# Optimization experiments

Hardware: AMD Instinct MI355X
Metric: run time of the kernel (lower is better)

Reference implementation:

```python
import jax, jax.numpy as jnp
import numpy as np

B, S, V, E, H, XD, C = 64, 512, 32000, 512, 1024, 512, 1024


def setup_inputs() -> dict:
    key = jax.random.key(0)
    ks = jax.random.split(key, 20)
    s = 0.02
    inp = {
        "X": jax.random.randint(ks[0], (B, S), 0, V),
        "h0": jax.random.normal(ks[1], (B, H), jnp.float32),
        "embed": jax.random.normal(ks[2], (V, E), jnp.float32) * s,
        "Wzh": jax.random.normal(ks[3], (H, H), jnp.float32) * s,
        "bzh": jnp.zeros((H,), jnp.float32),
        "Wzx": jax.random.normal(ks[4], (H, E), jnp.float32) * s,
        "bzx": jnp.zeros((H,), jnp.float32),
        "Wrh": jax.random.normal(ks[5], (H, H), jnp.float32) * s,
        "brh": jnp.zeros((H,), jnp.float32),
        "Wrx": jax.random.normal(ks[6], (H, E), jnp.float32) * s,
        "brx": jnp.zeros((H,), jnp.float32),
        "Wuh": jax.random.normal(ks[7], (H, H), jnp.float32) * s,
        "buh": jnp.zeros((H,), jnp.float32),
        "Wux": jax.random.normal(ks[8], (H, E), jnp.float32) * s,
        "bux": jnp.zeros((H,), jnp.float32),
        "Wxh": jax.random.normal(ks[9], (XD, H), jnp.float32) * s,
        "bxh": jnp.zeros((XD,), jnp.float32),
        "Wc": jax.random.normal(ks[10], (C, XD), jnp.float32) * s,
        "bc": jnp.zeros((C,), jnp.float32),
    }
    return inp


def reference(X, h0, embed, Wzh, bzh, Wzx, bzx, Wrh, brh, Wrx, brx,
              Wuh, buh, Wux, bux, Wxh, bxh, Wc, bc):
    x_embed = embed[X]                    # [B,S,E]
    xs = jnp.transpose(x_embed, (1, 0, 2))  # [S,B,E] for scan

    def step(ht, xt):
        zt = jax.nn.sigmoid(ht @ Wzh.T + bzh + xt @ Wzx.T + bzx)
        rt = jax.nn.sigmoid(ht @ Wrh.T + brh + xt @ Wrx.T + brx)
        ht_cand = jnp.tanh((rt * ht) @ Wuh.T + buh + xt @ Wux.T + bux)
        ht_new = (1.0 - zt) * ht + zt * ht_cand
        yt = ht_new @ Wxh.T + bxh          # [B,XD]
        yprob = yt @ Wc.T + bc             # [B,C]
        return ht_new, yprob

    _, yprobs = jax.lax.scan(step, h0, xs)  # [S,B,C]
    return jnp.transpose(yprobs, (1, 0, 2))  # [B,S,C]
```

## Files before the change

kernel.cpp:

```cpp
#include <hip/hip_runtime.h>

#define DEV __device__ __forceinline__

using bf16x8 = __attribute__((ext_vector_type(8))) short;
using u16x4  = __attribute__((ext_vector_type(4))) unsigned short;
using f32x4  = __attribute__((ext_vector_type(4))) float;

constexpr int B_ = 64, S_ = 512, V_ = 32000, E_ = 512, H_ = 1024, C_ = 1024;
constexpr int NWG = 128;
constexpr int JS  = 8;

constexpr size_t OFF_FH    = 0;
constexpr size_t OFF_FR    = 512;
constexpr size_t OFF_BIASG = 1024;
constexpr size_t OFF_BCOMB = OFF_BIASG + 3072*4;
constexpr size_t OFF_HB    = OFF_BCOMB + 1024*4;
constexpr size_t OFF_RHB   = OFF_HB + (size_t)B_*H_*2;
constexpr size_t OFF_WCOMB = OFF_RHB + (size_t)B_*H_*2;
constexpr size_t OFF_WXALL = OFF_WCOMB + (size_t)C_*H_*2;
constexpr size_t OFF_WZRF  = OFF_WXALL + (size_t)3072*512*2;
constexpr size_t OFF_WUF   = OFF_WZRF + (size_t)NWG*32768;
constexpr size_t OFF_EMB   = OFF_WUF + (size_t)NWG*16384;
constexpr size_t OFF_G     = OFF_EMB + (size_t)V_*E_*2;
constexpr size_t OFF_HS    = OFF_G + (size_t)S_*B_*3072*2;
constexpr size_t WS_NEED   = OFF_HS + (size_t)S_*B_*H_*2;

DEV unsigned short f2bf(float f){
  unsigned int x; __builtin_memcpy(&x, &f, 4);
  x += 0x7fffu + ((x>>16)&1u);
  return (unsigned short)(x>>16);
}
DEV float bf2f(unsigned short u){
  unsigned int x = ((unsigned int)u)<<16; float f; __builtin_memcpy(&f,&x,4); return f;
}

DEV int4 ld16_coh(const char* p){
  int4 r;
  asm volatile("global_load_dwordx4 %0, %1, off sc0 sc1" : "=v"(r) : "v"(p) : "memory");
  return r;
}
DEV void st16_coh(char* p, bf16x8 v){
  asm volatile("global_store_dwordx4 %0, %1, off sc0 sc1" :: "v"(p), "v"(v) : "memory");
}
DEV uint2 ld8_plain(const char* p){
  uint2 r;
  asm volatile("global_load_dwordx2 %0, %1, off" : "=v"(r) : "v"(p) : "memory");
  return r;
}

#define WAITVM(N) do{ asm volatile("s_waitcnt vmcnt(" #N ")" ::: "memory"); \
                      __builtin_amdgcn_sched_barrier(0); }while(0)

__global__ void k_cvt_embed(const float* __restrict__ src, unsigned short* __restrict__ dst){
  for (int i = blockIdx.x*blockDim.x + threadIdx.x; i < V_*E_; i += gridDim.x*blockDim.x)
    dst[i] = f2bf(src[i]);
}

__global__ void k_build_wx(const float* __restrict__ Wzx, const float* __restrict__ Wrx,
                           const float* __restrict__ Wux, unsigned short* __restrict__ out){
  for (int i = blockIdx.x*blockDim.x + threadIdx.x; i < 3072*512; i += gridDim.x*blockDim.x){
    int n = i>>9, k = i&511;
    int g = n>>10, r = n&1023;
    const float* W = (g==0) ? Wzx : (g==1) ? Wrx : Wux;
    out[i] = f2bf(W[(size_t)r*512 + k]);
  }
}

__global__ void k_biasg(const float* bzh, const float* bzx, const float* brh, const float* brx,
                        const float* buh, const float* bux, float* __restrict__ out){
  for (int i = blockIdx.x*blockDim.x + threadIdx.x; i < 3072; i += gridDim.x*blockDim.x){
    int g = i>>10, r = i&1023;
    float v = (g==0) ? (bzh[r]+bzx[r]) : (g==1) ? (brh[r]+brx[r]) : (buh[r]+bux[r]);
    out[i] = v;
  }
}

__global__ void k_frag(const float* __restrict__ Wa, const float* __restrict__ Wb,
                       unsigned short* __restrict__ out){
  for (int i = blockIdx.x*blockDim.x + threadIdx.x; i < NWG*32*64*8; i += gridDim.x*blockDim.x){
    int e  = i & 7;
    int l  = (i>>3) & 63;
    int ck = (i>>9) & 31;
    int wg = i>>14;
    int j  = l & 15;
    int k  = ck*32 + ((l>>4)<<3) + e;
    int row = wg*JS + (j&7);
    float v = (j < 8) ? Wa[(size_t)row*H_ + k] : Wb[(size_t)row*H_ + k];
    out[i] = f2bf(v);
  }
}

__global__ void k_frag2(const float* __restrict__ Wuh, unsigned short* __restrict__ out){
  for (int i = blockIdx.x*blockDim.x + threadIdx.x; i < NWG*32*32*8; i += gridDim.x*blockDim.x){
    int e=i&7, p=(i>>3)&31, ck=(i>>8)&31, wg=i>>13;
    int nn=p&7, h8=p>>3;
    out[i] = f2bf(Wuh[(size_t)(wg*8+nn)*H_ + ck*32 + h8*8 + e]);
  }
}

__global__ __launch_bounds__(256) void k_wcomb(const float* __restrict__ Wc,
                                               const float* __restrict__ Wxh,
                                               unsigned short* __restrict__ Wcomb){
  __shared__ float wc[16][512];
  const int c0 = blockIdx.x*16;
  const int tid = threadIdx.x;
  for (int q = tid; q < 16*512; q += 256)
    wc[q>>9][q&511] = Wc[(size_t)(c0 + (q>>9))*512 + (q&511)];
  __syncthreads();
  const int h4 = tid*4;
  f32x4 acc[16];
  #pragma unroll
  for (int ci=0; ci<16; ++ci) acc[ci] = (f32x4){0.f,0.f,0.f,0.f};
  for (int x=0; x<512; ++x){
    f32x4 wv = *(const f32x4*)(Wxh + (size_t)x*H_ + h4);
    #pragma unroll
    for (int ci=0; ci<16; ++ci) acc[ci] += wc[ci][x] * wv;
  }
  #pragma unroll
  for (int ci=0; ci<16; ++ci)
    #pragma unroll
    for (int e=0; e<4; ++e)
      Wcomb[(size_t)(c0+ci)*H_ + h4 + e] = f2bf(acc[ci][e]);
}

__global__ void k_bcomb(const float* __restrict__ Wc, const float* __restrict__ bxh,
                        const float* __restrict__ bc, float* __restrict__ out){
  int c = blockIdx.x*blockDim.x + threadIdx.x;
  if (c >= C_) return;
  float s = bc[c];
  for (int x=0; x<512; ++x) s += Wc[(size_t)c*512 + x]*bxh[x];
  out[c] = s;
}

__global__ void k_hinit(const float* __restrict__ h0, unsigned short* __restrict__ hbF){
  int i = blockIdx.x*256 + threadIdx.x;
  int e=i&7, l=(i>>3)&63, ck=(i>>9)&31, w=i>>14;
  hbF[i] = f2bf(h0[(size_t)(w*16+(l&15))*H_ + ck*32 + ((l>>4)<<3) + e]);
}

template<bool GATHER, int MODE>
__global__ __launch_bounds__(256) void gemm_bt(
  const unsigned short* __restrict__ Asrc, const int* __restrict__ Xidx,
  const unsigned short* __restrict__ embB,
  const unsigned short* __restrict__ Bw, const float* __restrict__ bias,
  void* __restrict__ Cout, int K, int KT, int NTN, int ldc)
{
  __shared__ unsigned short ldsA[128*64];
  __shared__ unsigned short ldsB[128*64];
  const int bid = blockIdx.x;
  const int tm = bid / NTN, tn = bid % NTN;
  const int m0 = tm*128, n0 = tn*128;
  const int tid = threadIdx.x, wave = tid>>6, lane = tid&63;
  const int wm = (wave&1)*64, wn = (wave>>1)*64;

  const char* srcA[4]; const char* srcB[4];
  int rr[4], cc[4];
  #pragma unroll
  for (int s=0; s<4; ++s){
    int L = s*4096 + tid*16;
    int r = L>>7, cb = L&127;
    rr[s]=r; cc[s]=cb;
    if constexpr (GATHER){
      int m = m0 + r; int tt = m>>6, bb = m&63;
      srcA[s] = (const char*)(embB + (size_t)Xidx[bb*S_ + tt]*(size_t)K);
    } else {
      srcA[s] = (const char*)(Asrc + (size_t)(m0+r)*(size_t)K);
    }
    srcB[s] = (const char*)(Bw + (size_t)(n0+r)*(size_t)K);
  }

  f32x4 acc[4][4];
  #pragma unroll
  for (int a=0;a<4;a++)
    #pragma unroll
    for (int b=0;b<4;b++) acc[a][b] = (f32x4){0.f,0.f,0.f,0.f};

  int4 ra[4], rb[4];
  auto loadRegs = [&](int kt){
    #pragma unroll
    for (int s=0;s<4;s++){
      ra[s] = *(const int4*)(srcA[s] + (size_t)kt*128 + cc[s]);
      rb[s] = *(const int4*)(srcB[s] + (size_t)kt*128 + cc[s]);
    }
  };
  auto writeLDS = [&](){
    #pragma unroll
    for (int s=0;s<4;s++){
      int off = (rr[s]<<7) + (cc[s] ^ ((rr[s]&7)<<4));
      *(int4*)((char*)ldsA + off) = ra[s];
      *(int4*)((char*)ldsB + off) = rb[s];
    }
  };

  loadRegs(0);
  for (int kt=0; kt<KT; ++kt){
    __syncthreads();
    writeLDS();
    if (kt+1 < KT) loadRegs(kt+1);
    __syncthreads();
    #pragma unroll
    for (int ck=0; ck<2; ++ck){
      bf16x8 af[4], bfr[4];
      #pragma unroll
      for (int q=0;q<4;q++){
        int ar = wm + q*16 + (lane&15);
        int ao = (ar<<7) + (((ck<<6) + ((lane>>4)<<4)) ^ ((ar&7)<<4));
        af[q] = *(const bf16x8*)((const char*)ldsA + ao);
        int br = wn + q*16 + (lane&15);
        int bo = (br<<7) + (((ck<<6) + ((lane>>4)<<4)) ^ ((br&7)<<4));
        bfr[q] = *(const bf16x8*)((const char*)ldsB + bo);
      }
      #pragma unroll
      for (int mi=0;mi<4;mi++)
        #pragma unroll
        for (int ni=0;ni<4;ni++)
          acc[mi][ni] = __builtin_amdgcn_mfma_f32_16x16x32_bf16(af[mi], bfr[ni], acc[mi][ni], 0,0,0);
    }
  }

  #pragma unroll
  for (int mi=0;mi<4;mi++){
    #pragma unroll
    for (int ni=0;ni<4;ni++){
      int gm = m0 + wm + mi*16 + ((lane>>4)<<2);
      int gn = n0 + wn + ni*16 + (lane&15);
      float bv = bias[gn];
      if constexpr (MODE == 1){
        #pragma unroll
        for (int r2=0;r2<4;r2++){
          float v = acc[mi][ni][r2] + bv;
          int m = gm + r2;
          ((float*)Cout)[ (size_t)((m&63)*S_ + (m>>6))*(size_t)ldc + gn ] = v;
        }
      } else {
        int t0 = gm>>6, b0 = gm&63;
        u16x4 pk;
        #pragma unroll
        for (int r2=0;r2<4;r2++) pk[r2] = f2bf(acc[mi][ni][r2] + bv);
        *(u16x4*)((unsigned short*)Cout + ((size_t)t0*3072 + gn)*64 + b0) = pk;
      }
    }
  }
}

DEV void pollge(const unsigned int* f, unsigned int p, int lane){
  const unsigned long long* q = (const unsigned long long*)f;
  int guard = 0;
  for(;;){
    unsigned long long v = __hip_atomic_load(&q[lane], __ATOMIC_RELAXED, __HIP_MEMORY_SCOPE_AGENT);
    bool ok = ((unsigned)v >= p) && ((unsigned)(v>>32) >= p);
    if (__all((int)ok)) break;
    __builtin_amdgcn_s_sleep(1);
    if (++guard > (1<<22)) break;
  }
}

__global__ __launch_bounds__(256) void k_scan(const float* __restrict__ h0, char* __restrict__ ws){
  const int wg = blockIdx.x;
  const int tid = threadIdx.x;
  const int wave = tid>>6, lane = tid&63;
  const int j0 = wg*JS;
  const int ckw = wg>>2, hiw = wg&3;

  unsigned int* fH = (unsigned int*)(ws + OFF_FH);
  unsigned int* fR = (unsigned int*)(ws + OFF_FR);
  char* hbF  = ws + OFF_HB;
  char* rhbF = ws + OFF_RHB;
  const unsigned short* G = (const unsigned short*)(ws + OFF_G);
  unsigned short* Hs  = (unsigned short*)(ws + OFF_HS);

  __shared__ __align__(16) char lds[32768 + 16384 + 1024 + 1024];
  char* f1  = lds;
  char* f2p = lds + 32768;
  unsigned short* tileA = (unsigned short*)(lds + 49152);
  unsigned short* tileB = (unsigned short*)(lds + 50176);

  {
    const int4* s1 = (const int4*)(ws + OFF_WZRF + (size_t)wg*32768);
    const int4* s2 = (const int4*)(ws + OFF_WUF  + (size_t)wg*16384);
    #pragma unroll
    for (int i=0;i<8;i++) ((int4*)f1)[tid + i*256] = s1[tid + i*256];
    #pragma unroll
    for (int i=0;i<4;i++) ((int4*)f2p)[tid + i*256] = s2[tid + i*256];
  }
  __syncthreads();

  const int n  = lane & 15;
  const int c  = n & 7;
  const bool isZ = (n < 8);
  const int hi2 = lane>>4;
  const int rbase = (wave<<4) + (hi2<<2);
  const int gcol = ((n>>3)<<10) + j0 + c;
  const int col2 = 2048 + j0 + c;

  float h_own[4];
  #pragma unroll
  for (int r2=0;r2<4;r2++)
    h_own[r2] = isZ ? h0[(size_t)(rbase+r2)*H_ + j0 + c] : 0.f;

  const char* myHb  = hbF  + ((size_t)wave<<15);
  const char* myRhb = rhbF + ((size_t)wave<<15);

#define LOAD8(buf, base, g0) { _Pragma("unroll") \
  for (int i=0;i<8;i++) buf[i] = ld16_coh((base) + ((((g0)*8+i)*64+lane)<<4)); }
#define MFMA8_1(buf, g0) { _Pragma("unroll") \
  for (int i=0;i<8;i++){ int ck=(g0)*8+i; \
    bf16x8 bv = *(const bf16x8*)(f1 + ((ck*64+lane)<<4)); \
    bf16x8 av = __builtin_bit_cast(bf16x8, buf[i]); \
    if (i&1) acc1 = __builtin_amdgcn_mfma_f32_16x16x32_bf16(av,bv,acc1,0,0,0); \
    else     acc0 = __builtin_amdgcn_mfma_f32_16x16x32_bf16(av,bv,acc0,0,0,0);} }
#define MFMA8_2(buf, g0) { _Pragma("unroll") \
  for (int i=0;i<8;i++){ int ck=(g0)*8+i; \
    bf16x8 bv = *(const bf16x8*)(f2p + ((ck*32 + hi2*8 + c)<<4)); \
    bf16x8 av = __builtin_bit_cast(bf16x8, buf[i]); \
    if (i&1) acc1 = __builtin_amdgcn_mfma_f32_16x16x32_bf16(av,bv,acc1,0,0,0); \
    else     acc0 = __builtin_amdgcn_mfma_f32_16x16x32_bf16(av,bv,acc0,0,0,0);} }

  for (int t=0; t<S_; ++t){
    uint2 gv1 = ld8_plain((const char*)(G + ((size_t)t*3072 + gcol)*64 + rbase));
    uint2 gv2 = ld8_plain((const char*)(G + ((size_t)t*3072 + col2)*64 + rbase));

    if (t > 0) pollge(fH, (unsigned)t, lane);
    WAITVM(0);

    f32x4 acc0 = (f32x4){0,0,0,0}, acc1 = (f32x4){0,0,0,0};
    {
      int4 bufA[8], bufB[8];
      LOAD8(bufA, myHb, 0);
      LOAD8(bufB, myHb, 1); WAITVM(8); MFMA8_1(bufA, 0);
      LOAD8(bufA, myHb, 2); WAITVM(8); MFMA8_1(bufB, 1);
      LOAD8(bufB, myHb, 3); WAITVM(8); MFMA8_1(bufA, 2);
      WAITVM(0);            MFMA8_1(bufB, 3);
    }
    f32x4 accs = acc0 + acc1;

    float zval[4];
    {
      unsigned short gu[4] = {(unsigned short)(gv1.x&0xffffu),(unsigned short)(gv1.x>>16),
                              (unsigned short)(gv1.y&0xffffu),(unsigned short)(gv1.y>>16)};
      #pragma unroll
      for (int r2=0;r2<4;r2++){
        float pre = accs[r2] + bf2f(gu[r2]);
        float sv = 1.f/(1.f + __expf(-pre));
        float hc = __shfl(h_own[r2], (lane & 48) | c, 64);
        zval[r2] = sv;
        if (!isZ) tileA[(wave*16 + hi2*4 + r2)*8 + c] = f2bf(sv*hc);
      }
    }
    __syncthreads();
    if (wave == 0){
      bf16x8 v = *(const bf16x8*)(tileA + lane*8);
      st16_coh(rhbF + ((((lane>>4)*32 + ckw)<<10) + (hiw<<8) + ((lane&15)<<4)), v);
      asm volatile("s_waitcnt vmcnt(0)" ::: "memory");
      if (lane == 0)
        __hip_atomic_store(&fR[wg], (unsigned)(t+1), __ATOMIC_RELAXED, __HIP_MEMORY_SCOPE_AGENT);
    }
    pollge(fR, (unsigned)(t+1), lane);
    WAITVM(0);

    acc0 = (f32x4){0,0,0,0}; acc1 = (f32x4){0,0,0,0};
    {
      int4 bufA[8], bufB[8];
      LOAD8(bufA, myRhb, 0);
      LOAD8(bufB, myRhb, 1); WAITVM(8); MFMA8_2(bufA, 0);
      LOAD8(bufA, myRhb, 2); WAITVM(8); MFMA8_2(bufB, 1);
      LOAD8(bufB, myRhb, 3); WAITVM(8); MFMA8_2(bufA, 2);
      WAITVM(0);             MFMA8_2(bufB, 3);
    }
    f32x4 acc2 = acc0 + acc1;

    if (isZ){
      unsigned short gu[4] = {(unsigned short)(gv2.x&0xffffu),(unsigned short)(gv2.x>>16),
                              (unsigned short)(gv2.y&0xffffu),(unsigned short)(gv2.y>>16)};
      #pragma unroll
      for (int r2=0;r2<4;r2++){
        float up = acc2[r2] + bf2f(gu[r2]);
        float e  = __expf(-2.f*up);
        float u  = (1.f - e)/(1.f + e);
        float hn = h_own[r2] + zval[r2]*(u - h_own[r2]);
        h_own[r2] = hn;
        tileB[(wave*16 + hi2*4 + r2)*8 + c] = f2bf(hn);
      }
    }
    __syncthreads();
    if (wave == 0){
      bf16x8 v = *(const bf16x8*)(tileB + lane*8);
      st16_coh(hbF + ((((lane>>4)*32 + ckw)<<10) + (hiw<<8) + ((lane&15)<<4)), v);
      *(bf16x8*)(Hs + (size_t)((t<<6) + lane)*H_ + j0) = v;
      asm volatile("s_waitcnt vmcnt(0)" ::: "memory");
      if (lane == 0)
        __hip_atomic_store(&fH[wg], (unsigned)(t+1), __ATOMIC_RELAXED, __HIP_MEMORY_SCOPE_AGENT);
    }
  }
#undef LOAD8
#undef MFMA8_1
#undef MFMA8_2
}

extern "C" void kernel_launch(void* const* d_in, const int* in_sizes, int n_in,
                              void* d_out, int out_size, void* d_ws, size_t ws_size,
                              hipStream_t stream)
{
  const int*   X    = (const int*)  d_in[0];
  const float* h0   = (const float*)d_in[1];
  const float* emb  = (const float*)d_in[2];
  const float* Wzh  = (const float*)d_in[3];
  const float* bzh  = (const float*)d_in[4];
  const float* Wzx  = (const float*)d_in[5];
  const float* bzx  = (const float*)d_in[6];
  const float* Wrh  = (const float*)d_in[7];
  const float* brh  = (const float*)d_in[8];
  const float* Wrx  = (const float*)d_in[9];
  const float* brx  = (const float*)d_in[10];
  const float* Wuh  = (const float*)d_in[11];
  const float* buh  = (const float*)d_in[12];
  const float* Wux  = (const float*)d_in[13];
  const float* bux  = (const float*)d_in[14];
  const float* Wxh  = (const float*)d_in[15];
  const float* bxh  = (const float*)d_in[16];
  const float* Wc   = (const float*)d_in[17];
  const float* bc   = (const float*)d_in[18];
  (void)in_sizes; (void)n_in;

  char* ws = (char*)d_ws;
  if (ws_size < WS_NEED){
    hipMemsetAsync(d_out, 0, (size_t)out_size*4, stream);
    return;
  }

  hipMemsetAsync(ws + OFF_FH, 0, 1024, stream);

  k_cvt_embed<<<4096, 256, 0, stream>>>(emb, (unsigned short*)(ws + OFF_EMB));
  k_build_wx <<<1536, 256, 0, stream>>>(Wzx, Wrx, Wux, (unsigned short*)(ws + OFF_WXALL));
  k_biasg    <<<12,   256, 0, stream>>>(bzh, bzx, brh, brx, buh, bux, (float*)(ws + OFF_BIASG));
  k_frag     <<<2048, 256, 0, stream>>>(Wzh, Wrh, (unsigned short*)(ws + OFF_WZRF));
  k_frag2    <<<1024, 256, 0, stream>>>(Wuh,      (unsigned short*)(ws + OFF_WUF));
  k_wcomb    <<<64,   256, 0, stream>>>(Wc, Wxh, (unsigned short*)(ws + OFF_WCOMB));
  k_bcomb    <<<4,    256, 0, stream>>>(Wc, bxh, bc, (float*)(ws + OFF_BCOMB));
  k_hinit    <<<256,  256, 0, stream>>>(h0, (unsigned short*)(ws + OFF_HB));

  gemm_bt<true,2><<<6144, 256, 0, stream>>>(
      nullptr, X, (const unsigned short*)(ws + OFF_EMB),
      (const unsigned short*)(ws + OFF_WXALL), (const float*)(ws + OFF_BIASG),
      (void*)(ws + OFF_G), 512, 8, 24, 3072);

  k_scan<<<NWG, 256, 0, stream>>>(h0, ws);

  gemm_bt<false,1><<<2048, 256, 0, stream>>>(
      (const unsigned short*)(ws + OFF_HS), nullptr, nullptr,
      (const unsigned short*)(ws + OFF_WCOMB), (const float*)(ws + OFF_BCOMB),
      d_out, 1024, 16, 8, 1024);
}
```

Measured before the change: 6.754 ms.

## Split scan into 512 single-wave workgroups with independent batch-quarter sync groups

The recurrent scan kernel goes from 128 four-wave workgroups to 512 single-wave workgroups, one per (column group, batch quarter). Each batch quarter now has its own flags and hidden-state buffers, so groups synchronise only with the 128 workgroups sharing their 16 batch rows. This removes the intra-block __syncthreads and the wave-0 serialised store, and shrinks each barrier's fan-in. In exchange each workgroup reloads the full 48KB weight fragment into LDS (4x total LDS footprint), and more workgroups spin-poll flags, which may increase memory traffic and require co-residency of 512 blocks.

```diff
diff --git a/kernel.cpp b/kernel.cpp
--- a/kernel.cpp
+++ b/kernel.cpp
@@ -7,20 +7,21 @@
 using f32x4  = __attribute__((ext_vector_type(4))) float;
 
 constexpr int B_ = 64, S_ = 512, V_ = 32000, E_ = 512, H_ = 1024, C_ = 1024;
-constexpr int NWG = 128;
+constexpr int NCG = 128;
+constexpr int NBG = 4;
 constexpr int JS  = 8;
 
 constexpr size_t OFF_FH    = 0;
-constexpr size_t OFF_FR    = 512;
-constexpr size_t OFF_BIASG = 1024;
+constexpr size_t OFF_FR    = 2048;
+constexpr size_t OFF_BIASG = 4096;
 constexpr size_t OFF_BCOMB = OFF_BIASG + 3072*4;
 constexpr size_t OFF_HB    = OFF_BCOMB + 1024*4;
-constexpr size_t OFF_RHB   = OFF_HB + (size_t)B_*H_*2;
-constexpr size_t OFF_WCOMB = OFF_RHB + (size_t)B_*H_*2;
+constexpr size_t OFF_RHB   = OFF_HB + (size_t)4*32768;
+constexpr size_t OFF_WCOMB = OFF_RHB + (size_t)4*32768;
 constexpr size_t OFF_WXALL = OFF_WCOMB + (size_t)C_*H_*2;
 constexpr size_t OFF_WZRF  = OFF_WXALL + (size_t)3072*512*2;
-constexpr size_t OFF_WUF   = OFF_WZRF + (size_t)NWG*32768;
-constexpr size_t OFF_EMB   = OFF_WUF + (size_t)NWG*16384;
+constexpr size_t OFF_WUF   = OFF_WZRF + (size_t)NCG*32768;
+constexpr size_t OFF_EMB   = OFF_WUF + (size_t)NCG*16384;
 constexpr size_t OFF_G     = OFF_EMB + (size_t)V_*E_*2;
 constexpr size_t OFF_HS    = OFF_G + (size_t)S_*B_*3072*2;
 constexpr size_t WS_NEED   = OFF_HS + (size_t)S_*B_*H_*2;
@@ -77,24 +78,24 @@
 
 __global__ void k_frag(const float* __restrict__ Wa, const float* __restrict__ Wb,
                        unsigned short* __restrict__ out){
-  for (int i = blockIdx.x*blockDim.x + threadIdx.x; i < NWG*32*64*8; i += gridDim.x*blockDim.x){
+  for (int i = blockIdx.x*blockDim.x + threadIdx.x; i < NCG*32*64*8; i += gridDim.x*blockDim.x){
     int e  = i & 7;
     int l  = (i>>3) & 63;
     int ck = (i>>9) & 31;
-    int wg = i>>14;
+    int g  = i>>14;
     int j  = l & 15;
     int k  = ck*32 + ((l>>4)<<3) + e;
-    int row = wg*JS + (j&7);
+    int row = g*JS + (j&7);
     float v = (j < 8) ? Wa[(size_t)row*H_ + k] : Wb[(size_t)row*H_ + k];
     out[i] = f2bf(v);
   }
 }
 
 __global__ void k_frag2(const float* __restrict__ Wuh, unsigned short* __restrict__ out){
-  for (int i = blockIdx.x*blockDim.x + threadIdx.x; i < NWG*32*32*8; i += gridDim.x*blockDim.x){
-    int e=i&7, p=(i>>3)&31, ck=(i>>8)&31, wg=i>>13;
+  for (int i = blockIdx.x*blockDim.x + threadIdx.x; i < NCG*32*32*8; i += gridDim.x*blockDim.x){
+    int e=i&7, p=(i>>3)&31, ck=(i>>8)&31, g=i>>13;
     int nn=p&7, h8=p>>3;
-    out[i] = f2bf(Wuh[(size_t)(wg*8+nn)*H_ + ck*32 + h8*8 + e]);
+    out[i] = f2bf(Wuh[(size_t)(g*8+nn)*H_ + ck*32 + h8*8 + e]);
   }
 }
 
@@ -134,8 +135,8 @@
 
 __global__ void k_hinit(const float* __restrict__ h0, unsigned short* __restrict__ hbF){
   int i = blockIdx.x*256 + threadIdx.x;
-  int e=i&7, l=(i>>3)&63, ck=(i>>9)&31, w=i>>14;
-  hbF[i] = f2bf(h0[(size_t)(w*16+(l&15))*H_ + ck*32 + ((l>>4)<<3) + e]);
+  int e=i&7, l=(i>>3)&63, ck=(i>>9)&31, q=i>>14;
+  hbF[i] = f2bf(h0[(size_t)(q*16+(l&15))*H_ + ck*32 + ((l>>4)<<3) + e]);
 }
 
 template<bool GATHER, int MODE>
@@ -255,41 +256,42 @@
   }
 }
 
-__global__ __launch_bounds__(256) void k_scan(const float* __restrict__ h0, char* __restrict__ ws){
-  const int wg = blockIdx.x;
-  const int tid = threadIdx.x;
-  const int wave = tid>>6, lane = tid&63;
-  const int j0 = wg*JS;
-  const int ckw = wg>>2, hiw = wg&3;
-
-  unsigned int* fH = (unsigned int*)(ws + OFF_FH);
-  unsigned int* fR = (unsigned int*)(ws + OFF_FR);
-  char* hbF  = ws + OFF_HB;
-  char* rhbF = ws + OFF_RHB;
+__global__ __launch_bounds__(64) void k_scan(const float* __restrict__ h0, char* __restrict__ ws){
+  const int Wid = blockIdx.x;
+  const int g = Wid & 127;
+  const int q = Wid >> 7;
+  const int lane = threadIdx.x;
+  const int j0 = g*JS;
+  const int b0 = q*16;
+
+  unsigned int* fH = (unsigned int*)(ws + OFF_FH) + q*128;
+  unsigned int* fR = (unsigned int*)(ws + OFF_FR) + q*128;
+  char* HF  = ws + OFF_HB  + (size_t)q*32768;
+  char* RHF = ws + OFF_RHB + (size_t)q*32768;
   const unsigned short* G = (const unsigned short*)(ws + OFF_G);
   unsigned short* Hs  = (unsigned short*)(ws + OFF_HS);
 
-  __shared__ __align__(16) char lds[32768 + 16384 + 1024 + 1024];
+  __shared__ __align__(16) char lds[32768 + 16384 + 512];
   char* f1  = lds;
   char* f2p = lds + 32768;
-  unsigned short* tileA = (unsigned short*)(lds + 49152);
-  unsigned short* tileB = (unsigned short*)(lds + 50176);
+  unsigned short* tA = (unsigned short*)(lds + 49152);
+  unsigned short* tB = (unsigned short*)(lds + 49152 + 256);
 
   {
-    const int4* s1 = (const int4*)(ws + OFF_WZRF + (size_t)wg*32768);
-    const int4* s2 = (const int4*)(ws + OFF_WUF  + (size_t)wg*16384);
-    #pragma unroll
-    for (int i=0;i<8;i++) ((int4*)f1)[tid + i*256] = s1[tid + i*256];
-    #pragma unroll
-    for (int i=0;i<4;i++) ((int4*)f2p)[tid + i*256] = s2[tid + i*256];
-  }
-  __syncthreads();
-
-  const int n  = lane & 15;
-  const int c  = n & 7;
+    const int4* s1 = (const int4*)(ws + OFF_WZRF + (size_t)g*32768);
+    const int4* s2 = (const int4*)(ws + OFF_WUF  + (size_t)g*16384);
+    #pragma unroll
+    for (int i=0;i<32;i++) ((int4*)f1)[lane + i*64]  = s1[lane + i*64];
+    #pragma unroll
+    for (int i=0;i<16;i++) ((int4*)f2p)[lane + i*64] = s2[lane + i*64];
+  }
+  asm volatile("s_waitcnt lgkmcnt(0)" ::: "memory");
+
+  const int n   = lane & 15;
+  const int c   = lane & 7;
   const bool isZ = (n < 8);
-  const int hi2 = lane>>4;
-  const int rbase = (wave<<4) + (hi2<<2);
+  const int hi4 = lane >> 4;
+  const int rbase = b0 + hi4*4;
   const int gcol = ((n>>3)<<10) + j0 + c;
   const int col2 = 2048 + j0 + c;
 
@@ -297,9 +299,6 @@
   #pragma unroll
   for (int r2=0;r2<4;r2++)
     h_own[r2] = isZ ? h0[(size_t)(rbase+r2)*H_ + j0 + c] : 0.f;
-
-  const char* myHb  = hbF  + ((size_t)wave<<15);
-  const char* myRhb = rhbF + ((size_t)wave<<15);
 
 #define LOAD8(buf, base, g0) { _Pragma("unroll") \
   for (int i=0;i<8;i++) buf[i] = ld16_coh((base) + ((((g0)*8+i)*64+lane)<<4)); }
@@ -311,7 +310,7 @@
     else     acc0 = __builtin_amdgcn_mfma_f32_16x16x32_bf16(av,bv,acc0,0,0,0);} }
 #define MFMA8_2(buf, g0) { _Pragma("unroll") \
   for (int i=0;i<8;i++){ int ck=(g0)*8+i; \
-    bf16x8 bv = *(const bf16x8*)(f2p + ((ck*32 + hi2*8 + c)<<4)); \
+    bf16x8 bv = *(const bf16x8*)(f2p + ((ck*32 + hi4*8 + c)<<4)); \
     bf16x8 av = __builtin_bit_cast(bf16x8, buf[i]); \
     if (i&1) acc1 = __builtin_amdgcn_mfma_f32_16x16x32_bf16(av,bv,acc1,0,0,0); \
     else     acc0 = __builtin_amdgcn_mfma_f32_16x16x32_bf16(av,bv,acc0,0,0,0);} }
@@ -321,16 +320,15 @@
     uint2 gv2 = ld8_plain((const char*)(G + ((size_t)t*3072 + col2)*64 + rbase));
 
     if (t > 0) pollge(fH, (unsigned)t, lane);
-    WAITVM(0);
 
     f32x4 acc0 = (f32x4){0,0,0,0}, acc1 = (f32x4){0,0,0,0};
     {
       int4 bufA[8], bufB[8];
-      LOAD8(bufA, myHb, 0);
-      LOAD8(bufB, myHb, 1); WAITVM(8); MFMA8_1(bufA, 0);
-      LOAD8(bufA, myHb, 2); WAITVM(8); MFMA8_1(bufB, 1);
-      LOAD8(bufB, myHb, 3); WAITVM(8); MFMA8_1(bufA, 2);
-      WAITVM(0);            MFMA8_1(bufB, 3);
+      LOAD8(bufA, HF, 0);
+      LOAD8(bufB, HF, 1); WAITVM(8); MFMA8_1(bufA, 0);
+      LOAD8(bufA, HF, 2); WAITVM(8); MFMA8_1(bufB, 1);
+      LOAD8(bufB, HF, 3); WAITVM(8); MFMA8_1(bufA, 2);
+      WAITVM(0);          MFMA8_1(bufB, 3);
     }
     f32x4 accs = acc0 + acc1;
 
@@ -342,30 +340,30 @@
       for (int r2=0;r2<4;r2++){
         float pre = accs[r2] + bf2f(gu[r2]);
         float sv = 1.f/(1.f + __expf(-pre));
-        float hc = __shfl(h_own[r2], (lane & 48) | c, 64);
+        float hc = __shfl_xor(h_own[r2], 8, 64);
         zval[r2] = sv;
-        if (!isZ) tileA[(wave*16 + hi2*4 + r2)*8 + c] = f2bf(sv*hc);
+        if (!isZ) tA[(hi4*4+r2)*8 + c] = f2bf(sv*hc);
       }
     }
-    __syncthreads();
-    if (wave == 0){
-      bf16x8 v = *(const bf16x8*)(tileA + lane*8);
-      st16_coh(rhbF + ((((lane>>4)*32 + ckw)<<10) + (hiw<<8) + ((lane&15)<<4)), v);
-      asm volatile("s_waitcnt vmcnt(0)" ::: "memory");
-      if (lane == 0)
-        __hip_atomic_store(&fR[wg], (unsigned)(t+1), __ATOMIC_RELAXED, __HIP_MEMORY_SCOPE_AGENT);
-    }
+    asm volatile("s_waitcnt lgkmcnt(0)" ::: "memory");
+    __builtin_amdgcn_sched_barrier(0);
+    if (lane < 16){
+      bf16x8 v = *(const bf16x8*)(tA + lane*8);
+      st16_coh(RHF + g*256 + lane*16, v);
+    }
+    WAITVM(0);
+    if (lane == 0)
+      __hip_atomic_store(&fR[g], (unsigned)(t+1), __ATOMIC_RELAXED, __HIP_MEMORY_SCOPE_AGENT);
     pollge(fR, (unsigned)(t+1), lane);
-    WAITVM(0);
 
     acc0 = (f32x4){0,0,0,0}; acc1 = (f32x4){0,0,0,0};
     {
       int4 bufA[8], bufB[8];
-      LOAD8(bufA, myRhb, 0);
-      LOAD8(bufB, myRhb, 1); WAITVM(8); MFMA8_2(bufA, 0);
-      LOAD8(bufA, myRhb, 2); WAITVM(8); MFMA8_2(bufB, 1);
-      LOAD8(bufB, myRhb, 3); WAITVM(8); MFMA8_2(bufA, 2);
-      WAITVM(0);             MFMA8_2(bufB, 3);
+      LOAD8(bufA, RHF, 0);
+      LOAD8(bufB, RHF, 1); WAITVM(8); MFMA8_2(bufA, 0);
+      LOAD8(bufA, RHF, 2); WAITVM(8); MFMA8_2(bufB, 1);
+      LOAD8(bufB, RHF, 3); WAITVM(8); MFMA8_2(bufA, 2);
+      WAITVM(0);           MFMA8_2(bufB, 3);
     }
     f32x4 acc2 = acc0 + acc1;
 
@@ -379,18 +377,19 @@
         float u  = (1.f - e)/(1.f + e);
         float hn = h_own[r2] + zval[r2]*(u - h_own[r2]);
         h_own[r2] = hn;
-        tileB[(wave*16 + hi2*4 + r2)*8 + c] = f2bf(hn);
+        tB[(hi4*4+r2)*8 + c] = f2bf(hn);
       }
     }
-    __syncthreads();
-    if (wave == 0){
-      bf16x8 v = *(const bf16x8*)(tileB + lane*8);
-      st16_coh(hbF + ((((lane>>4)*32 + ckw)<<10) + (hiw<<8) + ((lane&15)<<4)), v);
-      *(bf16x8*)(Hs + (size_t)((t<<6) + lane)*H_ + j0) = v;
-      asm volatile("s_waitcnt vmcnt(0)" ::: "memory");
-      if (lane == 0)
-        __hip_atomic_store(&fH[wg], (unsigned)(t+1), __ATOMIC_RELAXED, __HIP_MEMORY_SCOPE_AGENT);
-    }
+    asm volatile("s_waitcnt lgkmcnt(0)" ::: "memory");
+    __builtin_amdgcn_sched_barrier(0);
+    if (lane < 16){
+      bf16x8 v = *(const bf16x8*)(tB + lane*8);
+      *(bf16x8*)(Hs + (size_t)((t<<6) + b0 + lane)*H_ + j0) = v;
+      st16_coh(HF + g*256 + lane*16, v);
+    }
+    WAITVM(0);
+    if (lane == 0)
+      __hip_atomic_store(&fH[g], (unsigned)(t+1), __ATOMIC_RELAXED, __HIP_MEMORY_SCOPE_AGENT);
   }
 #undef LOAD8
 #undef MFMA8_1
@@ -428,7 +427,7 @@
     return;
   }
 
-  hipMemsetAsync(ws + OFF_FH, 0, 1024, stream);
+  hipMemsetAsync(ws + OFF_FH, 0, 4096, stream);
 
   k_cvt_embed<<<4096, 256, 0, stream>>>(emb, (unsigned short*)(ws + OFF_EMB));
   k_build_wx <<<1536, 256, 0, stream>>>(Wzx, Wrx, Wux, (unsigned short*)(ws + OFF_WXALL));
@@ -444,7 +443,7 @@
       (const unsigned short*)(ws + OFF_WXALL), (const float*)(ws + OFF_BIASG),
       (void*)(ws + OFF_G), 512, 8, 24, 3072);
 
-  k_scan<<<NWG, 256, 0, stream>>>(h0, ws);
+  k_scan<<<NCG*NBG, 64, 0, stream>>>(h0, ws);
 
   gemm_bt<false,1><<<2048, 256, 0, stream>>>(
       (const unsigned short*)(ws + OFF_HS), nullptr, nullptr,
```

After: 8.558 ms. +26.7%, slower.

## Replace block barriers with per-wave publishing and fetch-add counter flags

Applied to the files above, without the earlier changes.

Each wave now writes its own 16 rows of r*h and h to private LDS slices and publishes them to global memory itself. Each wave then bumps the workgroup flag with an atomic fetch-add, and pollers wait for four increments per step. This removes the two __syncthreads per timestep and the single-wave publish bottleneck. The change also issues all 32 coherent loads up front with staged waits, splits the MFMA chain across four accumulators, removes s_sleep from the poll loop and sets launch_bounds occupancy to 1. The cost is more atomics, more register pressure and busier polling traffic.

```diff
diff --git a/kernel.cpp b/kernel.cpp
--- a/kernel.cpp
+++ b/kernel.cpp
@@ -50,6 +50,8 @@
 
 #define WAITVM(N) do{ asm volatile("s_waitcnt vmcnt(" #N ")" ::: "memory"); \
                       __builtin_amdgcn_sched_barrier(0); }while(0)
+#define WAITLGKM() do{ asm volatile("s_waitcnt lgkmcnt(0)" ::: "memory"); \
+                       __builtin_amdgcn_sched_barrier(0); }while(0)
 
 __global__ void k_cvt_embed(const float* __restrict__ src, unsigned short* __restrict__ dst){
   for (int i = blockIdx.x*blockDim.x + threadIdx.x; i < V_*E_; i += gridDim.x*blockDim.x)
@@ -250,12 +252,11 @@
     unsigned long long v = __hip_atomic_load(&q[lane], __ATOMIC_RELAXED, __HIP_MEMORY_SCOPE_AGENT);
     bool ok = ((unsigned)v >= p) && ((unsigned)(v>>32) >= p);
     if (__all((int)ok)) break;
-    __builtin_amdgcn_s_sleep(1);
-    if (++guard > (1<<22)) break;
-  }
-}
-
-__global__ __launch_bounds__(256) void k_scan(const float* __restrict__ h0, char* __restrict__ ws){
+    if (++guard > (1<<24)) break;
+  }
+}
+
+__global__ __launch_bounds__(256,1) void k_scan(const float* __restrict__ h0, char* __restrict__ ws){
   const int wg = blockIdx.x;
   const int tid = threadIdx.x;
   const int wave = tid>>6, lane = tid&63;
@@ -269,11 +270,11 @@
   const unsigned short* G = (const unsigned short*)(ws + OFF_G);
   unsigned short* Hs  = (unsigned short*)(ws + OFF_HS);
 
-  __shared__ __align__(16) char lds[32768 + 16384 + 1024 + 1024];
+  __shared__ __align__(16) char lds[32768 + 16384 + 2048];
   char* f1  = lds;
   char* f2p = lds + 32768;
-  unsigned short* tileA = (unsigned short*)(lds + 49152);
-  unsigned short* tileB = (unsigned short*)(lds + 50176);
+  unsigned short* tAw = (unsigned short*)(lds + 49152 + wave*256);
+  unsigned short* tBw = (unsigned short*)(lds + 49152 + 1024 + wave*256);
 
   {
     const int4* s1 = (const int4*)(ws + OFF_WZRF + (size_t)wg*32768);
@@ -300,6 +301,8 @@
 
   const char* myHb  = hbF  + ((size_t)wave<<15);
   const char* myRhb = rhbF + ((size_t)wave<<15);
+  char* pubR = rhbF + ((size_t)wave<<15) + ((size_t)ckw<<10) + (hiw<<8);
+  char* pubH = hbF  + ((size_t)wave<<15) + ((size_t)ckw<<10) + (hiw<<8);
 
 #define LOAD8(buf, base, g0) { _Pragma("unroll") \
   for (int i=0;i<8;i++) buf[i] = ld16_coh((base) + ((((g0)*8+i)*64+lane)<<4)); }
@@ -307,32 +310,31 @@
   for (int i=0;i<8;i++){ int ck=(g0)*8+i; \
     bf16x8 bv = *(const bf16x8*)(f1 + ((ck*64+lane)<<4)); \
     bf16x8 av = __builtin_bit_cast(bf16x8, buf[i]); \
-    if (i&1) acc1 = __builtin_amdgcn_mfma_f32_16x16x32_bf16(av,bv,acc1,0,0,0); \
-    else     acc0 = __builtin_amdgcn_mfma_f32_16x16x32_bf16(av,bv,acc0,0,0,0);} }
+    accv[i&3] = __builtin_amdgcn_mfma_f32_16x16x32_bf16(av,bv,accv[i&3],0,0,0);} }
 #define MFMA8_2(buf, g0) { _Pragma("unroll") \
   for (int i=0;i<8;i++){ int ck=(g0)*8+i; \
     bf16x8 bv = *(const bf16x8*)(f2p + ((ck*32 + hi2*8 + c)<<4)); \
     bf16x8 av = __builtin_bit_cast(bf16x8, buf[i]); \
-    if (i&1) acc1 = __builtin_amdgcn_mfma_f32_16x16x32_bf16(av,bv,acc1,0,0,0); \
-    else     acc0 = __builtin_amdgcn_mfma_f32_16x16x32_bf16(av,bv,acc0,0,0,0);} }
+    accv[i&3] = __builtin_amdgcn_mfma_f32_16x16x32_bf16(av,bv,accv[i&3],0,0,0);} }
 
   for (int t=0; t<S_; ++t){
     uint2 gv1 = ld8_plain((const char*)(G + ((size_t)t*3072 + gcol)*64 + rbase));
     uint2 gv2 = ld8_plain((const char*)(G + ((size_t)t*3072 + col2)*64 + rbase));
 
-    if (t > 0) pollge(fH, (unsigned)t, lane);
-    WAITVM(0);
-
-    f32x4 acc0 = (f32x4){0,0,0,0}, acc1 = (f32x4){0,0,0,0};
+    if (t > 0) pollge(fH, 4u*(unsigned)t, lane);
+
+    f32x4 accv[4];
+    #pragma unroll
+    for (int a=0;a<4;a++) accv[a] = (f32x4){0,0,0,0};
     {
-      int4 bufA[8], bufB[8];
-      LOAD8(bufA, myHb, 0);
-      LOAD8(bufB, myHb, 1); WAITVM(8); MFMA8_1(bufA, 0);
-      LOAD8(bufA, myHb, 2); WAITVM(8); MFMA8_1(bufB, 1);
-      LOAD8(bufB, myHb, 3); WAITVM(8); MFMA8_1(bufA, 2);
-      WAITVM(0);            MFMA8_1(bufB, 3);
-    }
-    f32x4 accs = acc0 + acc1;
+      int4 b0[8], b1[8], b2[8], b3[8];
+      LOAD8(b0, myHb, 0); LOAD8(b1, myHb, 1); LOAD8(b2, myHb, 2); LOAD8(b3, myHb, 3);
+      WAITVM(24); MFMA8_1(b0, 0);
+      WAITVM(16); MFMA8_1(b1, 1);
+      WAITVM(8);  MFMA8_1(b2, 2);
+      WAITVM(0);  MFMA8_1(b3, 3);
+    }
+    f32x4 accs = (accv[0]+accv[1]) + (accv[2]+accv[3]);
 
     float zval[4];
     {
@@ -344,30 +346,30 @@
         float sv = 1.f/(1.f + __expf(-pre));
         float hc = __shfl(h_own[r2], (lane & 48) | c, 64);
         zval[r2] = sv;
-        if (!isZ) tileA[(wave*16 + hi2*4 + r2)*8 + c] = f2bf(sv*hc);
+        if (!isZ) tAw[(hi2*4 + r2)*8 + c] = f2bf(sv*hc);
       }
     }
-    __syncthreads();
-    if (wave == 0){
-      bf16x8 v = *(const bf16x8*)(tileA + lane*8);
-      st16_coh(rhbF + ((((lane>>4)*32 + ckw)<<10) + (hiw<<8) + ((lane&15)<<4)), v);
-      asm volatile("s_waitcnt vmcnt(0)" ::: "memory");
-      if (lane == 0)
-        __hip_atomic_store(&fR[wg], (unsigned)(t+1), __ATOMIC_RELAXED, __HIP_MEMORY_SCOPE_AGENT);
-    }
-    pollge(fR, (unsigned)(t+1), lane);
+    WAITLGKM();
+    if (lane < 16){
+      bf16x8 v = *(const bf16x8*)(tAw + lane*8);
+      st16_coh(pubR + (lane<<4), v);
+    }
     WAITVM(0);
-
-    acc0 = (f32x4){0,0,0,0}; acc1 = (f32x4){0,0,0,0};
+    if (lane == 0)
+      __hip_atomic_fetch_add(&fR[wg], 1u, __ATOMIC_RELAXED, __HIP_MEMORY_SCOPE_AGENT);
+    pollge(fR, 4u*(unsigned)(t+1), lane);
+
+    #pragma unroll
+    for (int a=0;a<4;a++) accv[a] = (f32x4){0,0,0,0};
     {
-      int4 bufA[8], bufB[8];
-      LOAD8(bufA, myRhb, 0);
-      LOAD8(bufB, myRhb, 1); WAITVM(8); MFMA8_2(bufA, 0);
-      LOAD8(bufA, myRhb, 2); WAITVM(8); MFMA8_2(bufB, 1);
-      LOAD8(bufB, myRhb, 3); WAITVM(8); MFMA8_2(bufA, 2);
-      WAITVM(0);             MFMA8_2(bufB, 3);
-    }
-    f32x4 acc2 = acc0 + acc1;
+      int4 b0[8], b1[8], b2[8], b3[8];
+      LOAD8(b0, myRhb, 0); LOAD8(b1, myRhb, 1); LOAD8(b2, myRhb, 2); LOAD8(b3, myRhb, 3);
+      WAITVM(24); MFMA8_2(b0, 0);
+      WAITVM(16); MFMA8_2(b1, 1);
+      WAITVM(8);  MFMA8_2(b2, 2);
+      WAITVM(0);  MFMA8_2(b3, 3);
+    }
+    f32x4 acc2 = (accv[0]+accv[1]) + (accv[2]+accv[3]);
 
     if (isZ){
       unsigned short gu[4] = {(unsigned short)(gv2.x&0xffffu),(unsigned short)(gv2.x>>16),
@@ -379,18 +381,18 @@
         float u  = (1.f - e)/(1.f + e);
         float hn = h_own[r2] + zval[r2]*(u - h_own[r2]);
         h_own[r2] = hn;
-        tileB[(wave*16 + hi2*4 + r2)*8 + c] = f2bf(hn);
+        tBw[(hi2*4 + r2)*8 + c] = f2bf(hn);
       }
     }
-    __syncthreads();
-    if (wave == 0){
-      bf16x8 v = *(const bf16x8*)(tileB + lane*8);
-      st16_coh(hbF + ((((lane>>4)*32 + ckw)<<10) + (hiw<<8) + ((lane&15)<<4)), v);
-      *(bf16x8*)(Hs + (size_t)((t<<6) + lane)*H_ + j0) = v;
-      asm volatile("s_waitcnt vmcnt(0)" ::: "memory");
-      if (lane == 0)
-        __hip_atomic_store(&fH[wg], (unsigned)(t+1), __ATOMIC_RELAXED, __HIP_MEMORY_SCOPE_AGENT);
-    }
+    WAITLGKM();
+    if (lane < 16){
+      bf16x8 v = *(const bf16x8*)(tBw + lane*8);
+      st16_coh(pubH + (lane<<4), v);
+      *(bf16x8*)(Hs + (size_t)((t<<6) + (wave<<4) + lane)*H_ + j0) = v;
+    }
+    WAITVM(0);
+    if (lane == 0)
+      __hip_atomic_fetch_add(&fH[wg], 1u, __ATOMIC_RELAXED, __HIP_MEMORY_SCOPE_AGENT);
   }
 #undef LOAD8
 #undef MFMA8_1
```

Result: slower. 14.94 ms (+121.2%).
